# Kernel tuning notes

Measured on AMD Instinct MI355X. Metric: run time of the kernel, lower is better.

The kernel has to match this reference:

```python
import jax, jax.numpy as jnp
import numpy as np

N_CODE = 1024
D_K = 512
K = 16
BETA = (0.25, 1.0)
N_SMAT = 2
N = 32768


def setup_inputs() -> dict:
    key = jax.random.key(0)
    k1, k2, k3, k4, k5, k6 = jax.random.split(key, 6)
    x = jax.random.normal(k1, (1, N, D_K), dtype=jnp.float32)
    c = jax.random.normal(k2, (N_CODE, D_K), dtype=jnp.float32)
    # trans linears: Linear(n_code, n_code // 2**i) for i = 1..n_smat
    s = 1.0 / np.sqrt(N_CODE)
    W1 = jax.random.uniform(k3, (N_CODE // 2, N_CODE), jnp.float32, -s, s)
    b1 = jax.random.uniform(k4, (N_CODE // 2,), jnp.float32, -s, s)
    W2 = jax.random.uniform(k5, (N_CODE // 4, N_CODE), jnp.float32, -s, s)
    b2 = jax.random.uniform(k6, (N_CODE // 4,), jnp.float32, -s, s)
    return {"x": x, "c": c, "W1": W1, "b1": b1, "W2": W2, "b2": b2,
            "training": 1, "get_k": 0}


def _quantize(x, cb):
    # argmin of squared euclidean distance == argmin of cdist (p=2)
    # d2[n, m] = ||x_n||^2 - 2 x_n . c_m + ||c_m||^2
    d2 = (jnp.sum(x * x, axis=1, keepdims=True)
          - 2.0 * (x @ cb.T)
          + jnp.sum(cb * cb, axis=1))
    z = jnp.argmin(d2, axis=1)
    return z, cb[z]


def _vq_loss(z_q, x):
    # mse(z_q, sg(x)) and mse(x, sg(z_q)); values identical in forward
    e = jnp.mean((z_q - x) ** 2)
    return BETA[0] * e + BETA[1] * e


def reference(x, c, W1, b1, W2, b2, training, get_k):
    x2 = x[0]  # squeeze(0) -> [N, d_k]

    main_z, main_z_q = _quantize(x2, c)

    # sub-scale codebooks: L(c.T).T == W @ c + b[:, None]
    sub_z_q = jnp.zeros_like(main_z_q)
    for W, b in ((W1, b1), (W2, b2)):
        sub_c = W @ c + b[:, None]  # [n_code // 2^i, d_k]
        _, sub_q = _quantize(x2, sub_c)
        sub_z_q = sub_z_q + sub_q
    sub_z_q = sub_z_q / N_SMAT

    if training:
        total_loss = _vq_loss(main_z_q, x2) + _vq_loss(sub_z_q, x2)
    else:
        total_loss = jnp.zeros(())

    # get_k=0 path: ms_k_i stays zeros
    ms_k_i = jnp.zeros((K, D_K), dtype=x2.dtype)

    # unique rows of main_z_q == number of distinct codebook indices used
    counts = jnp.zeros((N_CODE,), jnp.int32).at[main_z].add(1)
    unique_rows = jnp.sum(counts > 0)

    # straight-through (values unchanged in forward)
    main_out = (x2 + jax.lax.stop_gradient(main_z_q - x2))[None]
    sub_out = (x2 + jax.lax.stop_gradient(sub_z_q - x2))[None]
    return main_out, sub_out, total_loss, ms_k_i, unique_rows
```

## Files before the change

kernel.cpp:

```cpp
#include <hip/hip_runtime.h>
#include <cstdint>

typedef unsigned short ushort_t;
typedef unsigned int uint_t;
typedef _Float16 f16x8 __attribute__((ext_vector_type(8)));
typedef float f32x4 __attribute__((ext_vector_type(4)));

#define N_ROWS 32768
#define DK 512
#define NC_MAIN 1024
#define NCB 1792
#define NTILE 14
#define NBLK_RG 8192

#define MAIN_OFF 0
#define SUB_OFF  16777216
#define LOSS_OFF 33554432
#define MSK_OFF  33554433
#define UNIQ_OFF 33562625

__device__ __forceinline__ uint_t umin_(uint_t a, uint_t b) { return a < b ? a : b; }
__device__ __forceinline__ uint_t umax_(uint_t a, uint_t b) { return a > b ? a : b; }

__global__ __launch_bounds__(256) void build_subcb(
    const float* __restrict__ c, const float* __restrict__ W1,
    const float* __restrict__ b1, const float* __restrict__ W2,
    const float* __restrict__ b2, float* __restrict__ CB,
    _Float16* __restrict__ cbh)
{
    int tid = threadIdx.x;
    int tx = tid & 63, ty = tid >> 6;
    int col = blockIdx.x * 64 + tx;
    int row0 = blockIdx.y * 16 + ty * 4;
    if (row0 < 1024) {
#pragma unroll
        for (int r = 0; r < 4; ++r) {
            float v = c[(row0 + r) * DK + col];
            CB[(row0 + r) * DK + col] = v;
            cbh[(row0 + r) * DK + col] = (_Float16)v;
        }
    } else {
        int i0 = row0 - 1024;
        const float* W;
        const float* b;
        if (i0 < 512) { W = W1; b = b1; }
        else          { W = W2; b = b2; i0 -= 512; }
        float acc[4] = {0.f, 0.f, 0.f, 0.f};
#pragma unroll 8
        for (int j = 0; j < 1024; ++j) {
            float cv = c[j * DK + col];
#pragma unroll
            for (int r = 0; r < 4; ++r)
                acc[r] += W[(i0 + r) * 1024 + j] * cv;
        }
#pragma unroll
        for (int r = 0; r < 4; ++r) {
            float v = acc[r] + b[i0 + r];
            CB[(row0 + r) * DK + col] = v;
            cbh[(row0 + r) * DK + col] = (_Float16)v;
        }
    }
}

__global__ __launch_bounds__(64) void row_norms(const float* __restrict__ CB,
                                                float* __restrict__ norms) {
    int row = blockIdx.x;
    int lane = threadIdx.x;
    const float4* p = (const float4*)(CB + (size_t)row * DK);
    float s = 0.f;
#pragma unroll
    for (int i = lane; i < 128; i += 64) {
        float4 v = p[i];
        s += v.x * v.x + v.y * v.y + v.z * v.z + v.w * v.w;
    }
#pragma unroll
    for (int off = 32; off; off >>= 1) s += __shfl_down(s, off, 64);
    if (lane == 0) norms[row] = s;
}

__global__ __launch_bounds__(256) void cvt_x(const float* __restrict__ in,
                                             _Float16* __restrict__ out,
                                             int* __restrict__ used) {
    int i = blockIdx.x * 256 + threadIdx.x;
    if (i < 1024) used[i] = 0;
    const float4* p = (const float4*)in + (size_t)i * 2;
    float4 a = p[0], b = p[1];
    f16x8 o;
    o[0] = (_Float16)a.x; o[1] = (_Float16)a.y; o[2] = (_Float16)a.z; o[3] = (_Float16)a.w;
    o[4] = (_Float16)b.x; o[5] = (_Float16)b.y; o[6] = (_Float16)b.z; o[7] = (_Float16)b.w;
    *((f16x8*)out + i) = o;
}

__device__ __forceinline__ void async16(void* lds, const void* g) {
    __builtin_amdgcn_global_load_lds(
        (const __attribute__((address_space(1))) unsigned int*)(uintptr_t)g,
        (__attribute__((address_space(3))) unsigned int*)(uintptr_t)lds,
        16, 0, 0);
}

__global__ __launch_bounds__(256) void gemm_topk(
    const _Float16* __restrict__ xh, const _Float16* __restrict__ cbh,
    const float* __restrict__ norms, uint2* __restrict__ candbuf)
{
    __shared__ __align__(16) ushort_t As[2][128 * 32];
    __shared__ __align__(16) ushort_t Bs[2][128 * 32];
    __shared__ uint2 cand[128][2];

    const int tid = threadIdx.x;
    const int lane = tid & 63;
    const int wid = tid >> 6;
    const int wy = wid >> 1, wx = wid & 1;
    const int lane15 = lane & 15, q = lane >> 4;

    const int bid = blockIdx.y * NTILE + blockIdx.x;
    const int xcd = bid & 7;
    const int slot = bid >> 3;
    const int tileN = slot % NTILE;
    const int rowG = slot / NTILE;
    const int rowBase = (rowG * 8 + xcd) * 128;
    const int c0 = tileN * 128;

    size_t aoff[2], boff[2];
    int ldsoff[2];
#pragma unroll
    for (int i = 0; i < 2; ++i) {
        int gid = i * 256 + tid;
        int row = gid >> 2;
        int gp = gid & 3;
        int gsw = gp ^ (row & 3);
        aoff[i] = (size_t)(rowBase + row) * DK + gsw * 8;
        boff[i] = (size_t)(c0 + row) * DK + gsw * 8;
        ldsoff[i] = gid * 8;
    }

    int rA[4], rB[4];
#pragma unroll
    for (int t = 0; t < 4; ++t) {
        rA[t] = wy * 64 + t * 16 + lane15;
        rB[t] = wx * 64 + t * 16 + lane15;
    }

    f32x4 acc[4][4];
#pragma unroll
    for (int mr = 0; mr < 4; ++mr)
#pragma unroll
        for (int nc = 0; nc < 4; ++nc) acc[mr][nc] = (f32x4)0.f;

#pragma unroll
    for (int i = 0; i < 2; ++i) {
        async16(&As[0][ldsoff[i]], xh + aoff[i]);
        async16(&Bs[0][ldsoff[i]], cbh + boff[i]);
    }

#pragma unroll
    for (int it = 0; it < 16; ++it) {
        const int cur = it & 1;
        __syncthreads();
        if (it < 15) {
            const int nxt = cur ^ 1;
            const int kk = (it + 1) * 32;
#pragma unroll
            for (int i = 0; i < 2; ++i) {
                async16(&As[nxt][ldsoff[i]], xh + aoff[i] + kk);
                async16(&Bs[nxt][ldsoff[i]], cbh + boff[i] + kk);
            }
        }
        f16x8 av[4], bv[4];
#pragma unroll
        for (int mr = 0; mr < 4; ++mr)
            av[mr] = *(const f16x8*)&As[cur][rA[mr] * 32 + (q ^ (rA[mr] & 3)) * 8];
#pragma unroll
        for (int nc = 0; nc < 4; ++nc)
            bv[nc] = *(const f16x8*)&Bs[cur][rB[nc] * 32 + (q ^ (rB[nc] & 3)) * 8];
#pragma unroll
        for (int mr = 0; mr < 4; ++mr)
#pragma unroll
            for (int nc = 0; nc < 4; ++nc)
                acc[mr][nc] = __builtin_amdgcn_mfma_f32_16x16x32_f16(
                    av[mr], bv[nc], acc[mr][nc], 0, 0, 0);
    }

    float nrm[4];
    uint_t colGlob[4];
#pragma unroll
    for (int nc = 0; nc < 4; ++nc) {
        colGlob[nc] = (uint_t)(c0 + wx * 64 + nc * 16 + lane15);
        nrm[nc] = norms[colGlob[nc]];
    }

#pragma unroll
    for (int mr = 0; mr < 4; ++mr) {
#pragma unroll
        for (int r = 0; r < 4; ++r) {
            uint_t k[4];
#pragma unroll
            for (int nc = 0; nc < 4; ++nc) {
                float s = fmaf(-2.f, acc[mr][nc][r], nrm[nc]);
                uint_t b = __float_as_uint(s);
                uint_t u = b ^ ((uint_t)((int)b >> 31) | 0x80000000u);
                k[nc] = (u & 0xFFFFF800u) | colGlob[nc];
            }
            uint_t lo01 = umin_(k[0], k[1]), hi01 = umax_(k[0], k[1]);
            uint_t lo23 = umin_(k[2], k[3]), hi23 = umax_(k[2], k[3]);
            uint_t k1 = umin_(lo01, lo23);
            uint_t k2 = umin_(umin_(hi01, hi23), umax_(lo01, lo23));
#pragma unroll
            for (int m = 1; m <= 8; m <<= 1) {
                uint_t o1 = __shfl_xor(k1, m, 64);
                uint_t o2 = __shfl_xor(k2, m, 64);
                uint_t n1 = umin_(k1, o1);
                uint_t n2 = umin_(umax_(k1, o1), umin_(k2, o2));
                k1 = n1; k2 = n2;
            }
            if (lane15 == 0) {
                int rloc = wy * 64 + mr * 16 + q * 4 + r;
                cand[rloc][wx] = make_uint2(k1, k2);
            }
        }
    }
    __syncthreads();
    if (tid < 128) {
        uint2 a = cand[tid][0], b = cand[tid][1];
        uint_t k1 = umin_(a.x, b.x);
        uint_t k2 = umin_(umax_(a.x, b.x), umin_(a.y, b.y));
        candbuf[(size_t)(rowBase + tid) * NTILE + tileN] = make_uint2(k1, k2);
    }
}

__device__ __forceinline__ void push4u(uint_t v, uint_t* bs) {
#pragma unroll
    for (int j = 0; j < 4; ++j) {
        uint_t lo = umin_(v, bs[j]);
        uint_t hi = umax_(v, bs[j]);
        bs[j] = lo; v = hi;
    }
}

__global__ __launch_bounds__(256) void rescue_gather(
    const float* __restrict__ x, const float* __restrict__ CB,
    const float* __restrict__ norms, const uint2* __restrict__ candbuf,
    float* __restrict__ main_out, float* __restrict__ sub_out,
    float2* __restrict__ lossPart, int* __restrict__ used)
{
    const int lane = threadIdx.x & 63;
    const int wv = threadIdx.x >> 6;
    const int r = blockIdx.x * 4 + wv;

    const float4* xp = (const float4*)(x + (size_t)r * DK) + lane * 2;
    float4 xa = xp[0], xb = xp[1];

    const uint2* cbp = candbuf + (size_t)r * NTILE;

    int si[12];
    {
        uint_t bs[4];
#pragma unroll
        for (int j = 0; j < 4; ++j) bs[j] = 0xFFFFFFFFu;
#pragma unroll
        for (int t = 0; t < 8; ++t) {
            uint2 e = cbp[t];
            push4u(__builtin_amdgcn_readfirstlane(e.x), bs);
            push4u(__builtin_amdgcn_readfirstlane(e.y), bs);
        }
#pragma unroll
        for (int j = 0; j < 4; ++j) si[j] = (int)(bs[j] & 2047u);
#pragma unroll
        for (int j = 0; j < 4; ++j) bs[j] = 0xFFFFFFFFu;
#pragma unroll
        for (int t = 8; t < 12; ++t) {
            uint2 e = cbp[t];
            push4u(__builtin_amdgcn_readfirstlane(e.x), bs);
            push4u(__builtin_amdgcn_readfirstlane(e.y), bs);
        }
#pragma unroll
        for (int j = 0; j < 4; ++j) si[4 + j] = (int)(bs[j] & 2047u);
#pragma unroll
        for (int j = 0; j < 4; ++j) bs[j] = 0xFFFFFFFFu;
#pragma unroll
        for (int t = 12; t < 14; ++t) {
            uint2 e = cbp[t];
            push4u(__builtin_amdgcn_readfirstlane(e.x), bs);
            push4u(__builtin_amdgcn_readfirstlane(e.y), bs);
        }
#pragma unroll
        for (int j = 0; j < 4; ++j) si[8 + j] = (int)(bs[j] & 2047u);
    }

    float d[12];
#pragma unroll
    for (int k = 0; k < 12; ++k) {
        const float4* cp = (const float4*)(CB + (size_t)si[k] * DK) + lane * 2;
        float4 a = cp[0], b = cp[1];
        d[k] = xa.x * a.x + xa.y * a.y + xa.z * a.z + xa.w * a.w
             + xb.x * b.x + xb.y * b.y + xb.z * b.z + xb.w * b.w;
    }
#pragma unroll
    for (int off = 32; off; off >>= 1)
#pragma unroll
        for (int k = 0; k < 12; ++k) d[k] += __shfl_xor(d[k], off, 64);

    float sc[12];
#pragma unroll
    for (int k = 0; k < 12; ++k) sc[k] = norms[si[k]] - 2.f * d[k];

    int pick[3];
#pragma unroll
    for (int g = 0; g < 3; ++g) {
        float bv = sc[g * 4]; int bidx = si[g * 4];
#pragma unroll
        for (int k = 1; k < 4; ++k) {
            float v = sc[g * 4 + k]; int idx = si[g * 4 + k];
            if (v < bv || (v == bv && idx < bidx)) { bv = v; bidx = idx; }
        }
        pick[g] = bidx;
    }
    const int A = pick[0], B = pick[1], C = pick[2];

    const float4* pa = (const float4*)(CB + (size_t)A * DK) + lane * 2;
    const float4* pb = (const float4*)(CB + (size_t)B * DK) + lane * 2;
    const float4* pc = (const float4*)(CB + (size_t)C * DK) + lane * 2;
    float4* mo = (float4*)(main_out + (size_t)r * DK) + lane * 2;
    float4* so = (float4*)(sub_out + (size_t)r * DK) + lane * 2;
    float em = 0.f, es = 0.f;
#pragma unroll
    for (int i = 0; i < 2; ++i) {
        float4 xq = (i == 0) ? xa : xb;
        float4 cm = pa[i];
        float4 q1 = pb[i];
        float4 q2 = pc[i];
        float4 cs;
        cs.x = 0.5f * (q1.x + q2.x);
        cs.y = 0.5f * (q1.y + q2.y);
        cs.z = 0.5f * (q1.z + q2.z);
        cs.w = 0.5f * (q1.w + q2.w);
        mo[i] = cm;
        so[i] = cs;
        float t;
        t = cm.x - xq.x; em += t * t;
        t = cm.y - xq.y; em += t * t;
        t = cm.z - xq.z; em += t * t;
        t = cm.w - xq.w; em += t * t;
        t = cs.x - xq.x; es += t * t;
        t = cs.y - xq.y; es += t * t;
        t = cs.z - xq.z; es += t * t;
        t = cs.w - xq.w; es += t * t;
    }
#pragma unroll
    for (int off = 32; off; off >>= 1) {
        em += __shfl_down(em, off, 64);
        es += __shfl_down(es, off, 64);
    }
    __shared__ float sm[8];
    if (lane == 0) {
        sm[wv] = em; sm[4 + wv] = es;
        used[A] = 1;
    }
    __syncthreads();
    if (threadIdx.x == 0) {
        lossPart[blockIdx.x] = make_float2(sm[0] + sm[1] + sm[2] + sm[3],
                                           sm[4] + sm[5] + sm[6] + sm[7]);
    }
}

__global__ __launch_bounds__(256) void finalize_kernel(
    const int* __restrict__ used, const float2* __restrict__ lossPart,
    const int* __restrict__ training, float* __restrict__ out)
{
    int tid = threadIdx.x;
    int cnt = 0;
    for (int i = tid; i < 1024; i += 256) cnt += (used[i] != 0);
    float em = 0.f, es = 0.f;
    for (int i = tid; i < NBLK_RG; i += 256) {
        float2 p = lossPart[i];
        em += p.x; es += p.y;
    }
#pragma unroll
    for (int off = 32; off; off >>= 1) {
        cnt += __shfl_down(cnt, off, 64);
        em += __shfl_down(em, off, 64);
        es += __shfl_down(es, off, 64);
    }
    __shared__ int sc[4];
    __shared__ float se[4], ss[4];
    if ((tid & 63) == 0) { sc[tid >> 6] = cnt; se[tid >> 6] = em; ss[tid >> 6] = es; }
    __syncthreads();
    if (tid == 0) {
        int total = sc[0] + sc[1] + sc[2] + sc[3];
        float tl = 0.f;
        if (*training) {
            float l0 = se[0] + se[1] + se[2] + se[3];
            float l1 = ss[0] + ss[1] + ss[2] + ss[3];
            tl = 1.25f * (l0 + l1) * (1.0f / ((float)N_ROWS * (float)DK));
        }
        out[LOSS_OFF] = tl;
        out[UNIQ_OFF] = (float)total;
    }
    for (int i = tid; i < 8192; i += 256) out[MSK_OFF + i] = 0.f;
}

extern "C" void kernel_launch(void* const* d_in, const int* in_sizes, int n_in,
                              void* d_out, int out_size, void* d_ws, size_t ws_size,
                              hipStream_t stream) {
    const float* x = (const float*)d_in[0];
    const float* c = (const float*)d_in[1];
    const float* W1 = (const float*)d_in[2];
    const float* b1 = (const float*)d_in[3];
    const float* W2 = (const float*)d_in[4];
    const float* b2 = (const float*)d_in[5];
    const int* training = (const int*)d_in[6];
    float* out = (float*)d_out;

    char* p = (char*)d_ws;
    float* CB = (float*)p;          p += (size_t)NCB * DK * 4;
    _Float16* xh = (_Float16*)p;    p += (size_t)N_ROWS * DK * 2;
    _Float16* cbh = (_Float16*)p;   p += (size_t)NCB * DK * 2;
    uint2* candbuf = (uint2*)p;     p += (size_t)N_ROWS * NTILE * 8;
    float* norms = (float*)p;       p += NCB * 4;
    float2* lossPart = (float2*)p;  p += (size_t)NBLK_RG * 8;
    int* used = (int*)p;            p += 4096;

    build_subcb<<<dim3(8, 112), dim3(256), 0, stream>>>(c, W1, b1, W2, b2, CB, cbh);
    row_norms<<<dim3(NCB), dim3(64), 0, stream>>>(CB, norms);
    cvt_x<<<dim3(8192), dim3(256), 0, stream>>>(x, xh, used);
    gemm_topk<<<dim3(NTILE, 256), dim3(256), 0, stream>>>(xh, cbh, norms, candbuf);
    rescue_gather<<<dim3(NBLK_RG), dim3(256), 0, stream>>>(
        x, CB, norms, candbuf, out + MAIN_OFF, out + SUB_OFF, lossPart, used);
    finalize_kernel<<<dim3(1), dim3(256), 0, stream>>>(used, lossPart, training, out);
}
```

Measured before the change: 415.7 us.

## Enlarge GEMM tile to 256x256 with 8 waves and finer-grained software pipelining

The distance GEMM moves from 128x128 tiles with 4 waves to 256x256 tiles with 8 waves per block. It uses a deeper double-buffered LDS pipeline split into two k-halves, with explicit vmcnt/lgkmcnt waits, s_barrier phases, sched_barrier and setprio around the MFMA clusters. A new LDS swizzle is applied and the candidate scratch now reuses the A buffer. The larger tile raises arithmetic intensity and overlaps loads with MFMA, but it needs far more LDS and registers (acc[8][4]) and depends on fragile hand-tuned wait counts.

After: 433.4 us. +4.3%, slower.

```diff
diff --git a/kernel.cpp b/kernel.cpp
--- a/kernel.cpp
+++ b/kernel.cpp
@@ -98,87 +98,158 @@
         16, 0, 0);
 }
 
-__global__ __launch_bounds__(256) void gemm_topk(
+__global__ __launch_bounds__(512, 2) void gemm_topk(
     const _Float16* __restrict__ xh, const _Float16* __restrict__ cbh,
     const float* __restrict__ norms, uint2* __restrict__ candbuf)
 {
-    __shared__ __align__(16) ushort_t As[2][128 * 32];
-    __shared__ __align__(16) ushort_t Bs[2][128 * 32];
-    __shared__ uint2 cand[128][2];
+    __shared__ __align__(16) ushort_t As[2][2][256 * 32];
+    __shared__ __align__(16) ushort_t Bs[2][2][256 * 32];
 
     const int tid = threadIdx.x;
     const int lane = tid & 63;
     const int wid = tid >> 6;
-    const int wy = wid >> 1, wx = wid & 1;
+    const int wy = wid >> 2, wx = wid & 3;
     const int lane15 = lane & 15, q = lane >> 4;
 
-    const int bid = blockIdx.y * NTILE + blockIdx.x;
+    const int bid = blockIdx.x;
     const int xcd = bid & 7;
     const int slot = bid >> 3;
-    const int tileN = slot % NTILE;
-    const int rowG = slot / NTILE;
-    const int rowBase = (rowG * 8 + xcd) * 128;
-    const int c0 = tileN * 128;
+    const int tileP = slot % 7;
+    const int rowG = slot / 7;
+    const int rowBase = (rowG * 8 + xcd) * 256;
+    const int c0 = tileP * 256;
 
     size_t aoff[2], boff[2];
-    int ldsoff[2];
+    int ldsd[2];
 #pragma unroll
     for (int i = 0; i < 2; ++i) {
-        int gid = i * 256 + tid;
-        int row = gid >> 2;
-        int gp = gid & 3;
-        int gsw = gp ^ (row & 3);
-        aoff[i] = (size_t)(rowBase + row) * DK + gsw * 8;
-        boff[i] = (size_t)(c0 + row) * DK + gsw * 8;
-        ldsoff[i] = gid * 8;
-    }
-
-    int rA[4], rB[4];
-#pragma unroll
-    for (int t = 0; t < 4; ++t) {
-        rA[t] = wy * 64 + t * 16 + lane15;
-        rB[t] = wx * 64 + t * 16 + lane15;
-    }
-
-    f32x4 acc[4][4];
-#pragma unroll
-    for (int mr = 0; mr < 4; ++mr)
+        int d16 = i * 512 + tid;
+        int row = d16 >> 2, g = d16 & 3;
+        int srow = row ^ ((row >> 3) & 1);
+        int sg = g ^ ((row >> 1) & 3);
+        aoff[i] = (size_t)(rowBase + srow) * DK + (size_t)(sg * 8);
+        boff[i] = (size_t)(c0 + srow) * DK + (size_t)(sg * 8);
+        ldsd[i] = d16 * 8;
+    }
+
+#define STG_A(BUF, KS, KT) do { \
+        async16(&As[(BUF)][(KS)][ldsd[0]], xh + aoff[0] + (KT) * 64 + (KS) * 32); \
+        async16(&As[(BUF)][(KS)][ldsd[1]], xh + aoff[1] + (KT) * 64 + (KS) * 32); \
+    } while (0)
+#define STG_B(BUF, KS, KT) do { \
+        async16(&Bs[(BUF)][(KS)][ldsd[0]], cbh + boff[0] + (KT) * 64 + (KS) * 32); \
+        async16(&Bs[(BUF)][(KS)][ldsd[1]], cbh + boff[1] + (KT) * 64 + (KS) * 32); \
+    } while (0)
+
+    int rdA[8], rdB[4];
+#pragma unroll
+    for (int mr = 0; mr < 8; ++mr) {
+        int rl = wy * 128 + mr * 16 + lane15;
+        rdA[mr] = (rl ^ ((rl >> 3) & 1)) * 32 + (q ^ ((rl >> 1) & 3)) * 8;
+    }
+#pragma unroll
+    for (int nc = 0; nc < 4; ++nc) {
+        int cl = wx * 64 + nc * 16 + lane15;
+        rdB[nc] = (cl ^ ((cl >> 3) & 1)) * 32 + (q ^ ((cl >> 1) & 3)) * 8;
+    }
+
+    f32x4 acc[8][4];
+#pragma unroll
+    for (int mr = 0; mr < 8; ++mr)
 #pragma unroll
         for (int nc = 0; nc < 4; ++nc) acc[mr][nc] = (f32x4)0.f;
 
-#pragma unroll
-    for (int i = 0; i < 2; ++i) {
-        async16(&As[0][ldsoff[i]], xh + aoff[i]);
-        async16(&Bs[0][ldsoff[i]], cbh + boff[i]);
-    }
-
-#pragma unroll
-    for (int it = 0; it < 16; ++it) {
-        const int cur = it & 1;
-        __syncthreads();
-        if (it < 15) {
-            const int nxt = cur ^ 1;
-            const int kk = (it + 1) * 32;
-#pragma unroll
-            for (int i = 0; i < 2; ++i) {
-                async16(&As[nxt][ldsoff[i]], xh + aoff[i] + kk);
-                async16(&Bs[nxt][ldsoff[i]], cbh + boff[i] + kk);
-            }
-        }
-        f16x8 av[4], bv[4];
-#pragma unroll
-        for (int mr = 0; mr < 4; ++mr)
-            av[mr] = *(const f16x8*)&As[cur][rA[mr] * 32 + (q ^ (rA[mr] & 3)) * 8];
-#pragma unroll
-        for (int nc = 0; nc < 4; ++nc)
-            bv[nc] = *(const f16x8*)&Bs[cur][rB[nc] * 32 + (q ^ (rB[nc] & 3)) * 8];
+    STG_B(0, 0, 0); STG_A(0, 0, 0); STG_B(0, 1, 0); STG_A(0, 1, 0);
+    asm volatile("s_waitcnt vmcnt(4)" ::: "memory");
+    STG_B(1, 0, 1); STG_A(1, 0, 1); STG_B(1, 1, 1);
+    asm volatile("s_waitcnt vmcnt(6)" ::: "memory");
+    __builtin_amdgcn_s_barrier();
+
+    f16x8 av[4], bv[4];
+#pragma unroll
+    for (int t = 0; t < 8; ++t) {
+        const int b = t & 1;
+#pragma unroll
+        for (int nc = 0; nc < 4; ++nc) bv[nc] = *(const f16x8*)&Bs[b][0][rdB[nc]];
+#pragma unroll
+        for (int mr = 0; mr < 4; ++mr) av[mr] = *(const f16x8*)&As[b][0][rdA[mr]];
+        if (t + 1 < 8) STG_A(b ^ 1, 1, t + 1);
+        __builtin_amdgcn_sched_barrier(0);
+        __builtin_amdgcn_s_barrier();
+        asm volatile("s_waitcnt lgkmcnt(0)" ::: "memory");
+        __builtin_amdgcn_sched_barrier(0);
+        __builtin_amdgcn_s_setprio(1);
 #pragma unroll
         for (int mr = 0; mr < 4; ++mr)
 #pragma unroll
             for (int nc = 0; nc < 4; ++nc)
                 acc[mr][nc] = __builtin_amdgcn_mfma_f32_16x16x32_f16(
                     av[mr], bv[nc], acc[mr][nc], 0, 0, 0);
-    }
+        __builtin_amdgcn_s_setprio(0);
+        __builtin_amdgcn_sched_barrier(0);
+        __builtin_amdgcn_s_barrier();
+#pragma unroll
+        for (int mr = 0; mr < 4; ++mr) av[mr] = *(const f16x8*)&As[b][0][rdA[4 + mr]];
+        if (t + 2 < 8) STG_B(b, 0, t + 2);
+        __builtin_amdgcn_sched_barrier(0);
+        __builtin_amdgcn_s_barrier();
+        asm volatile("s_waitcnt lgkmcnt(0)" ::: "memory");
+        __builtin_amdgcn_sched_barrier(0);
+        __builtin_amdgcn_s_setprio(1);
+#pragma unroll
+        for (int mr = 0; mr < 4; ++mr)
+#pragma unroll
+            for (int nc = 0; nc < 4; ++nc)
+                acc[4 + mr][nc] = __builtin_amdgcn_mfma_f32_16x16x32_f16(
+                    av[mr], bv[nc], acc[4 + mr][nc], 0, 0, 0);
+        __builtin_amdgcn_s_setprio(0);
+        __builtin_amdgcn_sched_barrier(0);
+        __builtin_amdgcn_s_barrier();
+#pragma unroll
+        for (int nc = 0; nc < 4; ++nc) bv[nc] = *(const f16x8*)&Bs[b][1][rdB[nc]];
+#pragma unroll
+        for (int mr = 0; mr < 4; ++mr) av[mr] = *(const f16x8*)&As[b][1][rdA[mr]];
+        if (t + 2 < 8) STG_A(b, 0, t + 2);
+        __builtin_amdgcn_sched_barrier(0);
+        __builtin_amdgcn_s_barrier();
+        asm volatile("s_waitcnt lgkmcnt(0)" ::: "memory");
+        __builtin_amdgcn_sched_barrier(0);
+        __builtin_amdgcn_s_setprio(1);
+#pragma unroll
+        for (int mr = 0; mr < 4; ++mr)
+#pragma unroll
+            for (int nc = 0; nc < 4; ++nc)
+                acc[mr][nc] = __builtin_amdgcn_mfma_f32_16x16x32_f16(
+                    av[mr], bv[nc], acc[mr][nc], 0, 0, 0);
+        __builtin_amdgcn_s_setprio(0);
+        __builtin_amdgcn_sched_barrier(0);
+        __builtin_amdgcn_s_barrier();
+#pragma unroll
+        for (int mr = 0; mr < 4; ++mr) av[mr] = *(const f16x8*)&As[b][1][rdA[4 + mr]];
+        if (t + 2 < 8) STG_B(b, 1, t + 2);
+        __builtin_amdgcn_sched_barrier(0);
+        __builtin_amdgcn_s_barrier();
+        asm volatile("s_waitcnt lgkmcnt(0)" ::: "memory");
+        __builtin_amdgcn_sched_barrier(0);
+        __builtin_amdgcn_s_setprio(1);
+#pragma unroll
+        for (int mr = 0; mr < 4; ++mr)
+#pragma unroll
+            for (int nc = 0; nc < 4; ++nc)
+                acc[4 + mr][nc] = __builtin_amdgcn_mfma_f32_16x16x32_f16(
+                    av[mr], bv[nc], acc[4 + mr][nc], 0, 0, 0);
+        __builtin_amdgcn_s_setprio(0);
+        if (t < 7) {
+            if (t + 2 < 8) asm volatile("s_waitcnt vmcnt(6)" ::: "memory");
+            else           asm volatile("s_waitcnt vmcnt(0)" ::: "memory");
+        }
+        __builtin_amdgcn_sched_barrier(0);
+        __builtin_amdgcn_s_barrier();
+    }
+#undef STG_A
+#undef STG_B
+
+    uint2 (*cand)[4] = (uint2(*)[4])(void*)&As[0][0][0];
 
     float nrm[4];
     uint_t colGlob[4];
@@ -189,15 +260,15 @@
     }
 
 #pragma unroll
-    for (int mr = 0; mr < 4; ++mr) {
+    for (int mr = 0; mr < 8; ++mr) {
 #pragma unroll
         for (int r = 0; r < 4; ++r) {
             uint_t k[4];
 #pragma unroll
             for (int nc = 0; nc < 4; ++nc) {
                 float s = fmaf(-2.f, acc[mr][nc][r], nrm[nc]);
-                uint_t b = __float_as_uint(s);
-                uint_t u = b ^ ((uint_t)((int)b >> 31) | 0x80000000u);
+                uint_t bb = __float_as_uint(s);
+                uint_t u = bb ^ ((uint_t)((int)bb >> 31) | 0x80000000u);
                 k[nc] = (u & 0xFFFFF800u) | colGlob[nc];
             }
             uint_t lo01 = umin_(k[0], k[1]), hi01 = umax_(k[0], k[1]);
@@ -213,17 +284,20 @@
                 k1 = n1; k2 = n2;
             }
             if (lane15 == 0) {
-                int rloc = wy * 64 + mr * 16 + q * 4 + r;
+                int rloc = wy * 128 + mr * 16 + q * 4 + r;
                 cand[rloc][wx] = make_uint2(k1, k2);
             }
         }
     }
     __syncthreads();
-    if (tid < 128) {
-        uint2 a = cand[tid][0], b = cand[tid][1];
-        uint_t k1 = umin_(a.x, b.x);
-        uint_t k2 = umin_(umax_(a.x, b.x), umin_(a.y, b.y));
-        candbuf[(size_t)(rowBase + tid) * NTILE + tileN] = make_uint2(k1, k2);
+    {
+        int half = tid >> 8;
+        int row = tid & 255;
+        uint2 a = cand[row][half * 2], b2 = cand[row][half * 2 + 1];
+        uint_t k1 = umin_(a.x, b2.x);
+        uint_t k2 = umin_(umax_(a.x, b2.x), umin_(a.y, b2.y));
+        candbuf[(size_t)(rowBase + row) * NTILE + (tileP * 2 + half)] =
+            make_uint2(k1, k2);
     }
 }
 
@@ -422,7 +496,7 @@
     build_subcb<<<dim3(8, 112), dim3(256), 0, stream>>>(c, W1, b1, W2, b2, CB, cbh);
     row_norms<<<dim3(NCB), dim3(64), 0, stream>>>(CB, norms);
     cvt_x<<<dim3(8192), dim3(256), 0, stream>>>(x, xh, used);
-    gemm_topk<<<dim3(NTILE, 256), dim3(256), 0, stream>>>(xh, cbh, norms, candbuf);
+    gemm_topk<<<dim3(896), dim3(512), 0, stream>>>(xh, cbh, norms, candbuf);
     rescue_gather<<<dim3(NBLK_RG), dim3(256), 0, stream>>>(
         x, CB, norms, candbuf, out + MAIN_OFF, out + SUB_OFF, lossPart, used);
     finalize_kernel<<<dim3(1), dim3(256), 0, stream>>>(used, lossPart, training, out);
```

## Compute each 128x128 GEMM tile with a single wave instead of four

Applied to the files above, without the earlier changes.

Each gemm_topk block now holds one 64-lane wave that computes the full 128x128 tile with an 8x8 MFMA accumulator array. It stages all tile loads itself, waits on vmcnt instead of __syncthreads, and writes candidates straight to global memory, which removes the shared-memory cross-wave merge. This cuts block barriers and gives each fragment more register reuse. In exchange it needs 256 accumulator registers per lane and has far fewer waves per CU to hide latency, and the LDS read swizzle changes.

Measured after the change: 428.8 us. 1.03x slower.

```diff
diff --git a/kernel.cpp b/kernel.cpp
--- a/kernel.cpp
+++ b/kernel.cpp
@@ -98,112 +98,95 @@
         16, 0, 0);
 }
 
-__global__ __launch_bounds__(256) void gemm_topk(
+__global__ __launch_bounds__(64, 1) void gemm_topk(
     const _Float16* __restrict__ xh, const _Float16* __restrict__ cbh,
     const float* __restrict__ norms, uint2* __restrict__ candbuf)
 {
     __shared__ __align__(16) ushort_t As[2][128 * 32];
     __shared__ __align__(16) ushort_t Bs[2][128 * 32];
-    __shared__ uint2 cand[128][2];
-
-    const int tid = threadIdx.x;
-    const int lane = tid & 63;
-    const int wid = tid >> 6;
-    const int wy = wid >> 1, wx = wid & 1;
+
+    const int lane = threadIdx.x;
     const int lane15 = lane & 15, q = lane >> 4;
 
-    const int bid = blockIdx.y * NTILE + blockIdx.x;
+    const int bid = blockIdx.x;
     const int xcd = bid & 7;
     const int slot = bid >> 3;
     const int tileN = slot % NTILE;
-    const int rowG = slot / NTILE;
-    const int rowBase = (rowG * 8 + xcd) * 128;
+    const int rowT = (slot / NTILE) * 8 + xcd;
+    const int rowBase = rowT * 128;
     const int c0 = tileN * 128;
 
-    size_t aoff[2], boff[2];
-    int ldsoff[2];
-#pragma unroll
-    for (int i = 0; i < 2; ++i) {
-        int gid = i * 256 + tid;
-        int row = gid >> 2;
-        int gp = gid & 3;
-        int gsw = gp ^ (row & 3);
-        aoff[i] = (size_t)(rowBase + row) * DK + gsw * 8;
-        boff[i] = (size_t)(c0 + row) * DK + gsw * 8;
-        ldsoff[i] = gid * 8;
-    }
-
-    int rA[4], rB[4];
-#pragma unroll
-    for (int t = 0; t < 4; ++t) {
-        rA[t] = wy * 64 + t * 16 + lane15;
-        rB[t] = wx * 64 + t * 16 + lane15;
-    }
-
-    f32x4 acc[4][4];
-#pragma unroll
-    for (int mr = 0; mr < 4; ++mr)
-#pragma unroll
-        for (int nc = 0; nc < 4; ++nc) acc[mr][nc] = (f32x4)0.f;
-
-#pragma unroll
-    for (int i = 0; i < 2; ++i) {
-        async16(&As[0][ldsoff[i]], xh + aoff[i]);
-        async16(&Bs[0][ldsoff[i]], cbh + boff[i]);
-    }
-
-#pragma unroll
-    for (int it = 0; it < 16; ++it) {
-        const int cur = it & 1;
-        __syncthreads();
-        if (it < 15) {
-            const int nxt = cur ^ 1;
-            const int kk = (it + 1) * 32;
-#pragma unroll
-            for (int i = 0; i < 2; ++i) {
-                async16(&As[nxt][ldsoff[i]], xh + aoff[i] + kk);
-                async16(&Bs[nxt][ldsoff[i]], cbh + boff[i] + kk);
-            }
-        }
-        f16x8 av[4], bv[4];
-#pragma unroll
-        for (int mr = 0; mr < 4; ++mr)
-            av[mr] = *(const f16x8*)&As[cur][rA[mr] * 32 + (q ^ (rA[mr] & 3)) * 8];
-#pragma unroll
-        for (int nc = 0; nc < 4; ++nc)
-            bv[nc] = *(const f16x8*)&Bs[cur][rB[nc] * 32 + (q ^ (rB[nc] & 3)) * 8];
-#pragma unroll
-        for (int mr = 0; mr < 4; ++mr)
-#pragma unroll
-            for (int nc = 0; nc < 4; ++nc)
+    const int srow = lane >> 2;
+    const int sg = (lane & 3) ^ ((lane >> 3) & 3);
+    const size_t aO = (size_t)(rowBase + srow) * DK + (size_t)(sg * 8);
+    const size_t bO = (size_t)(c0 + srow) * DK + (size_t)(sg * 8);
+    const int ldsg = lane * 8;
+
+#define STG(BUF, KT) do { \
+    _Pragma("unroll") \
+    for (int i_ = 0; i_ < 8; ++i_) { \
+        async16(&As[(BUF)][ldsg + i_ * 512], xh  + aO + (size_t)i_ * (16 * DK) + (KT) * 32); \
+        async16(&Bs[(BUF)][ldsg + i_ * 512], cbh + bO + (size_t)i_ * (16 * DK) + (KT) * 32); \
+    } } while (0)
+
+    const int rbase = lane15 * 32 + ((q ^ ((lane15 >> 1) & 3)) * 8);
+
+    f32x4 acc[8][8];
+#pragma unroll
+    for (int mr = 0; mr < 8; ++mr)
+#pragma unroll
+        for (int nc = 0; nc < 8; ++nc) acc[mr][nc] = (f32x4)0.f;
+
+    STG(0, 0);
+#pragma unroll
+    for (int kt = 0; kt < 16; ++kt) {
+        const int b = kt & 1;
+        if (kt < 15) {
+            STG(b ^ 1, kt + 1);
+            asm volatile("s_waitcnt vmcnt(16)" ::: "memory");
+        } else {
+            asm volatile("s_waitcnt vmcnt(0)" ::: "memory");
+        }
+        __builtin_amdgcn_sched_barrier(0);
+        f16x8 av[8], bv[8];
+#pragma unroll
+        for (int mr = 0; mr < 8; ++mr)
+            av[mr] = *(const f16x8*)&As[b][mr * 512 + rbase];
+#pragma unroll
+        for (int nc = 0; nc < 8; ++nc)
+            bv[nc] = *(const f16x8*)&Bs[b][nc * 512 + rbase];
+#pragma unroll
+        for (int mr = 0; mr < 8; ++mr)
+#pragma unroll
+            for (int nc = 0; nc < 8; ++nc)
                 acc[mr][nc] = __builtin_amdgcn_mfma_f32_16x16x32_f16(
                     av[mr], bv[nc], acc[mr][nc], 0, 0, 0);
     }
-
-    float nrm[4];
-    uint_t colGlob[4];
-#pragma unroll
-    for (int nc = 0; nc < 4; ++nc) {
-        colGlob[nc] = (uint_t)(c0 + wx * 64 + nc * 16 + lane15);
-        nrm[nc] = norms[colGlob[nc]];
-    }
-
-#pragma unroll
-    for (int mr = 0; mr < 4; ++mr) {
+#undef STG
+
+    float nrm[8];
+    uint_t colG[8];
+#pragma unroll
+    for (int nc = 0; nc < 8; ++nc) {
+        colG[nc] = (uint_t)(c0 + nc * 16 + lane15);
+        nrm[nc] = norms[colG[nc]];
+    }
+
+#pragma unroll
+    for (int mr = 0; mr < 8; ++mr) {
 #pragma unroll
         for (int r = 0; r < 4; ++r) {
-            uint_t k[4];
-#pragma unroll
-            for (int nc = 0; nc < 4; ++nc) {
+            uint_t k1 = 0xFFFFFFFFu, k2 = 0xFFFFFFFFu;
+#pragma unroll
+            for (int nc = 0; nc < 8; ++nc) {
                 float s = fmaf(-2.f, acc[mr][nc][r], nrm[nc]);
-                uint_t b = __float_as_uint(s);
-                uint_t u = b ^ ((uint_t)((int)b >> 31) | 0x80000000u);
-                k[nc] = (u & 0xFFFFF800u) | colGlob[nc];
+                uint_t bb = __float_as_uint(s);
+                uint_t u = bb ^ ((uint_t)((int)bb >> 31) | 0x80000000u);
+                uint_t k = (u & 0xFFFFF800u) | colG[nc];
+                uint_t n1 = umin_(k1, k);
+                k2 = umin_(k2, umax_(k1, k));
+                k1 = n1;
             }
-            uint_t lo01 = umin_(k[0], k[1]), hi01 = umax_(k[0], k[1]);
-            uint_t lo23 = umin_(k[2], k[3]), hi23 = umax_(k[2], k[3]);
-            uint_t k1 = umin_(lo01, lo23);
-            uint_t k2 = umin_(umin_(hi01, hi23), umax_(lo01, lo23));
 #pragma unroll
             for (int m = 1; m <= 8; m <<= 1) {
                 uint_t o1 = __shfl_xor(k1, m, 64);
@@ -213,17 +196,10 @@
                 k1 = n1; k2 = n2;
             }
             if (lane15 == 0) {
-                int rloc = wy * 64 + mr * 16 + q * 4 + r;
-                cand[rloc][wx] = make_uint2(k1, k2);
+                int grow = rowBase + mr * 16 + q * 4 + r;
+                candbuf[(size_t)grow * NTILE + tileN] = make_uint2(k1, k2);
             }
         }
-    }
-    __syncthreads();
-    if (tid < 128) {
-        uint2 a = cand[tid][0], b = cand[tid][1];
-        uint_t k1 = umin_(a.x, b.x);
-        uint_t k2 = umin_(umax_(a.x, b.x), umin_(a.y, b.y));
-        candbuf[(size_t)(rowBase + tid) * NTILE + tileN] = make_uint2(k1, k2);
     }
 }
 
@@ -422,7 +398,7 @@
     build_subcb<<<dim3(8, 112), dim3(256), 0, stream>>>(c, W1, b1, W2, b2, CB, cbh);
     row_norms<<<dim3(NCB), dim3(64), 0, stream>>>(CB, norms);
     cvt_x<<<dim3(8192), dim3(256), 0, stream>>>(x, xh, used);
-    gemm_topk<<<dim3(NTILE, 256), dim3(256), 0, stream>>>(xh, cbh, norms, candbuf);
+    gemm_topk<<<dim3(3584), dim3(64), 0, stream>>>(xh, cbh, norms, candbuf);
     rescue_gather<<<dim3(NBLK_RG), dim3(256), 0, stream>>>(
         x, CB, norms, candbuf, out + MAIN_OFF, out + SUB_OFF, lossPart, used);
     finalize_kernel<<<dim3(1), dim3(256), 0, stream>>>(used, lossPart, training, out);
```
